# Kernel tuning notes

Hardware: AMD Instinct MI355X
Metric: run time of the kernel (lower is better)

The kernel has to match this reference:

```python
import jax, jax.numpy as jnp
import numpy as np
import math

HIDDEN = 2048
N_HEADS = 16
N_KV = 8
HEAD_DIM = 128
EPS = 1e-6
THETA = 1000000.0
B, S = 1, 2048


def rotate_half(x):
    x1, x2 = jnp.split(x, 2, axis=-1)
    return jnp.concatenate((-x2, x1), axis=-1)


def rms_norm(x, w, eps=EPS):
    xf = x.astype(jnp.float32)
    var = jnp.mean(xf * xf, axis=-1, keepdims=True)
    return (w * (xf * jax.lax.rsqrt(var + eps)).astype(x.dtype))


def setup_inputs() -> dict:
    key = jax.random.key(0)
    ks = jax.random.split(key, 8)
    hidden_states = jax.random.normal(ks[0], (B, S, HIDDEN), dtype=jnp.float32)
    # additive causal mask: 0 on/below diagonal, -1e9 above
    causal = jnp.triu(jnp.full((S, S), -1e9, dtype=jnp.float32), k=1)
    attention_mask = causal[None, None, :, :]
    position_ids = jnp.arange(S, dtype=jnp.int64 if jax.config.jax_enable_x64 else jnp.int32)[None, :]
    sc = 0.02
    wq = jax.random.normal(ks[1], (N_HEADS * HEAD_DIM, HIDDEN), dtype=jnp.float32) * sc
    wk = jax.random.normal(ks[2], (N_KV * HEAD_DIM, HIDDEN), dtype=jnp.float32) * sc
    wv = jax.random.normal(ks[3], (N_KV * HEAD_DIM, HIDDEN), dtype=jnp.float32) * sc
    wo = jax.random.normal(ks[4], (HIDDEN, N_HEADS * HEAD_DIM), dtype=jnp.float32) * sc
    q_norm_w = jnp.ones((HEAD_DIM,), dtype=jnp.float32)
    k_norm_w = jnp.ones((HEAD_DIM,), dtype=jnp.float32)
    return {"hidden_states": hidden_states, "attention_mask": attention_mask,
            "position_ids": position_ids, "wq": wq, "wk": wk, "wv": wv,
            "wo": wo, "q_norm_w": q_norm_w, "k_norm_w": k_norm_w}


def reference(hidden_states, attention_mask, position_ids, wq, wk, wv, wo, q_norm_w, k_norm_w):
    b, s, _ = hidden_states.shape
    # projections (nn.Linear: x @ W^T)
    q = (hidden_states @ wq.T).reshape(b, s, N_HEADS, HEAD_DIM).transpose(0, 2, 1, 3)   # [b,h,s,d]
    k = (hidden_states @ wk.T).reshape(b, s, N_KV, HEAD_DIM).transpose(0, 2, 1, 3)      # [b,kv,s,d]
    v = (hidden_states @ wv.T).reshape(b, s, N_KV, HEAD_DIM).transpose(0, 2, 1, 3)
    # rotary embedding
    inv_freq = 1.0 / (THETA ** (jnp.arange(0, HEAD_DIM, 2, dtype=jnp.float32) / HEAD_DIM))  # [d/2]
    freqs = position_ids.astype(jnp.float32)[:, :, None] * inv_freq[None, None, :]          # [b,s,d/2]
    emb = jnp.concatenate((freqs, freqs), axis=-1)                                          # [b,s,d]
    cos = jnp.cos(emb)[:, None, :, :].astype(hidden_states.dtype)                           # [b,1,s,d]
    sin = jnp.sin(emb)[:, None, :, :].astype(hidden_states.dtype)
    q = q * cos + rotate_half(q) * sin
    k = k * cos + rotate_half(k) * sin
    # per-head QK RMSNorm (applied AFTER RoPE, matching source)
    q = rms_norm(q, q_norm_w)
    k = rms_norm(k, k_norm_w)
    # GQA repeat kv heads
    n_rep = N_HEADS // N_KV
    k = jnp.repeat(k, n_rep, axis=1)  # [b,h,s,d]
    v = jnp.repeat(v, n_rep, axis=1)
    # attention
    scores = jnp.einsum('bhqd,bhkd->bhqk', q, k) / math.sqrt(HEAD_DIM)
    scores = scores + attention_mask
    probs = jax.nn.softmax(scores.astype(jnp.float32), axis=-1).astype(q.dtype)
    ctx = jnp.einsum('bhqk,bhkd->bhqd', probs, v)
    ctx = ctx.transpose(0, 2, 1, 3).reshape(b, s, N_HEADS * HEAD_DIM)
    return ctx @ wo.T
```

## Files before the change

kernel.cpp:

```cpp
#include <hip/hip_runtime.h>
#include <hip/hip_bf16.h>

#define HIDDEN   2048
#define N_HEADS  16
#define N_KV     8
#define HEAD_DIM 128
#define SEQ      2048
#define EPS      1e-6f

#define BM 128
#define BN 128
#define BK 32

#define ATQ 64
#define ATK 64
#define QKS 136
#define VTS 72

typedef __hip_bfloat16 bf16;
typedef __bf16  bf16x8 __attribute__((ext_vector_type(8)));
typedef short   short8 __attribute__((ext_vector_type(8)));
typedef short   short4v __attribute__((ext_vector_type(4)));
typedef float   f32x4  __attribute__((ext_vector_type(4)));

typedef __attribute__((address_space(1))) void gvoid;
typedef __attribute__((address_space(3))) void lvoid;

#define ASYNC16(g, l) \
    __builtin_amdgcn_global_load_lds((gvoid*)(g), (lvoid*)(l), 16, 0, 0)

__device__ __forceinline__ short f2bfbits(float x) {
    union { bf16 h; short s; } u;
    u.h = __float2bfloat16(x);
    return u.s;
}

__global__ __launch_bounds__(256) void cvt_bf16(const float4* __restrict__ src,
                                                short4v* __restrict__ dst, int n4) {
    const int i = blockIdx.x * 256 + threadIdx.x;
    if (i >= n4) return;
    const float4 v = src[i];
    short4v p;
    p[0] = f2bfbits(v.x); p[1] = f2bfbits(v.y);
    p[2] = f2bfbits(v.z); p[3] = f2bfbits(v.w);
    dst[i] = p;
}

template <int MODE>
__device__ __forceinline__ void gemm_bf(const bf16* __restrict__ A,
                                        const bf16* __restrict__ B,
                                        float* __restrict__ C,
                                        bf16* __restrict__ Ct,
                                        int K, int ldc, int bm, int bn) {
    __shared__ __align__(16) short As[BM * BK];
    __shared__ __align__(16) short Bs[BN * BK];
    const int tid  = threadIdx.x;
    const int lane = tid & 63;
    const int wave = tid >> 6;
    const int wy   = wave & 1;
    const int wx   = wave >> 1;
    const int lrow = lane & 15;
    const int lk   = lane >> 4;
    const int srow = tid >> 2;
    const int scol = (tid & 3) * 8;

    f32x4 acc[4][4] = {};

    for (int k0 = 0; k0 < K; k0 += BK) {
        #pragma unroll
        for (int r = 0; r < 2; r++) {
            const int row = r * 64 + srow;
            ASYNC16(&A[(size_t)(bm + row) * K + k0 + scol],
                    &As[(r * 64 + wave * 16) * BK]);
            ASYNC16(&B[(size_t)(bn + row) * K + k0 + scol],
                    &Bs[(r * 64 + wave * 16) * BK]);
        }
        __syncthreads();

        short8 af[4], bfr[4];
        #pragma unroll
        for (int i = 0; i < 4; i++) {
            af[i]  = *(const short8*)&As[(wy * 64 + i * 16 + lrow) * BK + lk * 8];
            bfr[i] = *(const short8*)&Bs[(wx * 64 + i * 16 + lrow) * BK + lk * 8];
        }
        #pragma unroll
        for (int i = 0; i < 4; i++)
            #pragma unroll
            for (int j = 0; j < 4; j++)
                acc[i][j] = __builtin_amdgcn_mfma_f32_16x16x32_bf16(
                    __builtin_bit_cast(bf16x8, af[i]),
                    __builtin_bit_cast(bf16x8, bfr[j]), acc[i][j], 0, 0, 0);
        __syncthreads();
    }

    #pragma unroll
    for (int i = 0; i < 4; i++)
        #pragma unroll
        for (int j = 0; j < 4; j++) {
            if (MODE == 0) {
                #pragma unroll
                for (int v = 0; v < 4; v++)
                    C[(size_t)(bm + wy * 64 + i * 16 + lk * 4 + v) * ldc
                      + bn + wx * 64 + j * 16 + lrow] = acc[i][j][v];
            } else {
                short4v pk;
                #pragma unroll
                for (int v = 0; v < 4; v++) pk[v] = f2bfbits(acc[i][j][v]);
                *(short4v*)&Ct[(size_t)(bn + wx * 64 + j * 16 + lrow) * ldc
                               + bm + wy * 64 + i * 16 + lk * 4] = pk;
            }
        }
}

__global__ __launch_bounds__(256) void qkv_mfma(const bf16* __restrict__ x,
                                                const bf16* __restrict__ wq,
                                                const bf16* __restrict__ wk,
                                                const bf16* __restrict__ wv,
                                                float* __restrict__ Q,
                                                float* __restrict__ Kc,
                                                bf16* __restrict__ Vt) {
    const int by = blockIdx.y;
    const int bm = blockIdx.x * 128;
    if (by < 16)
        gemm_bf<0>(x, wq, Q, nullptr, HIDDEN, 2048, bm, by * 128);
    else if (by < 24)
        gemm_bf<0>(x, wk, Kc, nullptr, HIDDEN, 1024, bm, (by - 16) * 128);
    else
        gemm_bf<1>(x, wv, nullptr, Vt, HIDDEN, SEQ, bm, (by - 24) * 128);
}

__global__ __launch_bounds__(256) void oproj_mfma(const bf16* __restrict__ ctx,
                                                  const bf16* __restrict__ wo,
                                                  float* __restrict__ out) {
    gemm_bf<0>(ctx, wo, out, nullptr, N_HEADS * HEAD_DIM, HIDDEN,
               blockIdx.x * 128, blockIdx.y * 128);
}

__global__ __launch_bounds__(256) void rope_norm_kernel(
        const float* __restrict__ Q, const float* __restrict__ K,
        bf16* __restrict__ Qbf, bf16* __restrict__ Kbf,
        const float* __restrict__ qw, const float* __restrict__ kw) {
    const int s = blockIdx.x;
    const int h = blockIdx.y * 4 + (threadIdx.x >> 6);
    const int l = threadIdx.x & 63;

    const float* src;
    const float* w;
    if (h < N_HEADS) { src = Q + (size_t)s * (N_HEADS * HEAD_DIM) + h * HEAD_DIM; w = qw; }
    else             { src = K + (size_t)s * (N_KV * HEAD_DIM) + (h - N_HEADS) * HEAD_DIM; w = kw; }

    const float x1 = src[l];
    const float x2 = src[l + 64];
    const float inv_freq = exp2f((float)l * (-19.931568569324174f / 64.0f));
    const float ang = (float)s * inv_freq;
    float sn, cs;
    __sincosf(ang, &sn, &cs);
    float r1 = x1 * cs - x2 * sn;
    float r2 = x2 * cs + x1 * sn;

    float ss = r1 * r1 + r2 * r2;
    #pragma unroll
    for (int off = 1; off < 64; off <<= 1)
        ss += __shfl_xor(ss, off, 64);
    const float rs = rsqrtf(ss / 128.0f + EPS);

    if (h < N_HEADS) {
        bf16* dst = Qbf + ((size_t)s * N_HEADS + h) * HEAD_DIM;
        dst[l]      = __float2bfloat16(w[l] * r1 * rs);
        dst[l + 64] = __float2bfloat16(w[l + 64] * r2 * rs);
    } else {
        bf16* dst = Kbf + ((size_t)s * N_KV + (h - N_HEADS)) * HEAD_DIM;
        dst[l]      = __float2bfloat16(w[l] * r1 * rs);
        dst[l + 64] = __float2bfloat16(w[l + 64] * r2 * rs);
    }
}

__global__ __launch_bounds__(256) void attn_mfma(bf16* __restrict__ QC,
                                                 const bf16* __restrict__ KbfG,
                                                 const bf16* __restrict__ VtG) {
    const int h     = blockIdx.y;
    const int px    = (int)((blockIdx.x * 13u) & 31u);
    const int qtile = (h < 8) ? px : 31 - px;
    const int q0    = qtile * ATQ;
    const int kvh   = h >> 1;
    const int tid   = threadIdx.x;
    const int lane  = tid & 63;
    const int w     = tid >> 6;
    const int lrow  = lane & 15;
    const int lk    = lane >> 4;
    const float scale = 0.08838834764831845f;

    __shared__ short Ks[ATK * QKS];
    __shared__ short Vt[HEAD_DIM * VTS];
    __shared__ short Ps[ATQ * VTS];

    f32x4 O[8] = {};
    float m_run[4] = {-1e30f, -1e30f, -1e30f, -1e30f};
    float l_run[4] = {};

    short8 aq[4];
    {
        const bf16* qrow =
            &QC[(size_t)(q0 + w * 16 + lrow) * (N_HEADS * HEAD_DIM) + h * HEAD_DIM];
        #pragma unroll
        for (int kc = 0; kc < 4; kc++)
            aq[kc] = *(const short8*)&qrow[kc * 32 + lk * 8];
    }

    for (int t = 0; t <= qtile; t++) {
        const int k0 = t * ATK;
        for (int idx = tid; idx < ATK * 16; idx += 256) {
            const int r = idx >> 4, c8 = idx & 15;
            *(short8*)&Ks[r * QKS + c8 * 8] = *(const short8*)
                &KbfG[((size_t)(k0 + r) * N_KV + kvh) * HEAD_DIM + c8 * 8];
        }
        for (int idx = tid; idx < HEAD_DIM * 8; idx += 256) {
            const int d = idx >> 3, ck = idx & 7;
            *(short8*)&Vt[d * VTS + ck * 8] =
                *(const short8*)&VtG[((size_t)kvh * HEAD_DIM + d) * SEQ + k0 + ck * 8];
        }
        __syncthreads();

        f32x4 s[4] = {};
        #pragma unroll
        for (int nt = 0; nt < 4; nt++)
            #pragma unroll
            for (int kc = 0; kc < 4; kc++) {
                const short8 bk = *(const short8*)
                    &Ks[(nt * 16 + lrow) * QKS + kc * 32 + lk * 8];
                s[nt] = __builtin_amdgcn_mfma_f32_16x16x32_bf16(
                    __builtin_bit_cast(bf16x8, aq[kc]),
                    __builtin_bit_cast(bf16x8, bk), s[nt], 0, 0, 0);
            }

        float p[4][4];
        float mloc[4] = {-1e30f, -1e30f, -1e30f, -1e30f};
        #pragma unroll
        for (int nt = 0; nt < 4; nt++) {
            const int kglob = k0 + nt * 16 + lrow;
            #pragma unroll
            for (int r = 0; r < 4; r++) {
                float v = s[nt][r] * scale;
                v = (kglob <= q0 + w * 16 + lk * 4 + r) ? v : -1e30f;
                p[nt][r] = v;
                mloc[r] = fmaxf(mloc[r], v);
            }
        }
        #pragma unroll
        for (int off = 1; off < 16; off <<= 1)
            #pragma unroll
            for (int r = 0; r < 4; r++)
                mloc[r] = fmaxf(mloc[r], __shfl_xor(mloc[r], off, 64));

        float alpha[4], ls[4];
        #pragma unroll
        for (int r = 0; r < 4; r++) {
            const float mnew = fmaxf(m_run[r], mloc[r]);
            alpha[r] = __expf(m_run[r] - mnew);
            m_run[r] = mnew;
            ls[r] = 0.f;
        }
        #pragma unroll
        for (int nt = 0; nt < 4; nt++)
            #pragma unroll
            for (int r = 0; r < 4; r++) {
                const float e = __expf(p[nt][r] - m_run[r]);
                Ps[(w * 16 + lk * 4 + r) * VTS + nt * 16 + lrow] = f2bfbits(e);
                ls[r] += e;
            }
        #pragma unroll
        for (int off = 1; off < 16; off <<= 1)
            #pragma unroll
            for (int r = 0; r < 4; r++)
                ls[r] += __shfl_xor(ls[r], off, 64);
        #pragma unroll
        for (int r = 0; r < 4; r++)
            l_run[r] = l_run[r] * alpha[r] + ls[r];
        #pragma unroll
        for (int dnt = 0; dnt < 8; dnt++)
            #pragma unroll
            for (int r = 0; r < 4; r++)
                O[dnt][r] *= alpha[r];

        __syncthreads();

        short8 pa[2];
        #pragma unroll
        for (int ks = 0; ks < 2; ks++)
            pa[ks] = *(const short8*)&Ps[(w * 16 + lrow) * VTS + ks * 32 + lk * 8];
        #pragma unroll
        for (int dnt = 0; dnt < 8; dnt++)
            #pragma unroll
            for (int ks = 0; ks < 2; ks++) {
                const short8 vb = *(const short8*)
                    &Vt[(dnt * 16 + lrow) * VTS + ks * 32 + lk * 8];
                O[dnt] = __builtin_amdgcn_mfma_f32_16x16x32_bf16(
                    __builtin_bit_cast(bf16x8, pa[ks]),
                    __builtin_bit_cast(bf16x8, vb), O[dnt], 0, 0, 0);
            }
        __syncthreads();
    }

    #pragma unroll
    for (int r = 0; r < 4; r++) {
        const float invl = 1.0f / l_run[r];
        bf16* orow = &QC[(size_t)(q0 + w * 16 + lk * 4 + r) * (N_HEADS * HEAD_DIM)
                         + h * HEAD_DIM];
        #pragma unroll
        for (int dnt = 0; dnt < 8; dnt++)
            orow[dnt * 16 + lrow] = __float2bfloat16(O[dnt][r] * invl);
    }
}

extern "C" void kernel_launch(void* const* d_in, const int* in_sizes, int n_in,
                              void* d_out, int out_size, void* d_ws, size_t ws_size,
                              hipStream_t stream) {
    const float* x   = (const float*)d_in[0];
    const float* wq  = (const float*)d_in[3];
    const float* wk  = (const float*)d_in[4];
    const float* wv  = (const float*)d_in[5];
    const float* wo  = (const float*)d_in[6];
    const float* qnw = (const float*)d_in[7];
    const float* knw = (const float*)d_in[8];

    char*  ws   = (char*)d_ws;
    float* Qw   = (float*)ws;
    bf16*  xbf  = (bf16*)(ws + (16u << 20));
    bf16*  wqbf = (bf16*)(ws + (24u << 20));
    bf16*  wobf = wqbf;
    bf16*  wkbf = (bf16*)(ws + (32u << 20));
    bf16*  wvbf = (bf16*)(ws + (36u << 20));
    bf16*  Qbf  = (bf16*)(ws + (40u << 20));
    float* Kb   = (float*)d_out;
    bf16*  VtG  = (bf16*)((char*)d_out + (8u << 20));
    bf16*  KbfG = (bf16*)((char*)d_out + (12u << 20));

    cvt_bf16<<<4096, 256, 0, stream>>>((const float4*)x,  (short4v*)xbf,  1048576);
    cvt_bf16<<<4096, 256, 0, stream>>>((const float4*)wq, (short4v*)wqbf, 1048576);
    cvt_bf16<<<2048, 256, 0, stream>>>((const float4*)wk, (short4v*)wkbf, 524288);
    cvt_bf16<<<2048, 256, 0, stream>>>((const float4*)wv, (short4v*)wvbf, 524288);

    qkv_mfma<<<dim3(SEQ / 128, 32), 256, 0, stream>>>(xbf, wqbf, wkbf, wvbf,
                                                      Qw, Kb, VtG);

    cvt_bf16<<<4096, 256, 0, stream>>>((const float4*)wo, (short4v*)wobf, 1048576);

    rope_norm_kernel<<<dim3(SEQ, 6), 256, 0, stream>>>(Qw, Kb, Qbf, KbfG, qnw, knw);

    attn_mfma<<<dim3(SEQ / ATQ, N_HEADS), 256, 0, stream>>>(Qbf, KbfG, VtG);

    oproj_mfma<<<dim3(SEQ / 128, HIDDEN / 128), 256, 0, stream>>>(Qbf, wobf,
                                                                  (float*)d_out);
}
```

Baseline: 375.4 us.

## Split causal attention over KV range for long query tiles and combine partials

Query tiles in the second half of the sequence now have their KV loop split into two chunks handled by separate blocks, giving 48 blocks per head instead of 32 with a max of 16 KV tiles each. Each block writes unnormalized fp32 partial outputs plus running max and sum, and a new combine kernel merges them with log-sum-exp rescaling and writes bf16 context. This targets the load imbalance and tail of the causal attention grid, at the cost of an extra launch and fp32 partial-output traffic through the workspace.

```diff
diff --git a/kernel.cpp b/kernel.cpp
--- a/kernel.cpp
+++ b/kernel.cpp
@@ -16,6 +16,7 @@
 #define ATK 64
 #define QKS 136
 #define VTS 72
+#define CHUNK 16
 
 typedef __hip_bfloat16 bf16;
 typedef __bf16  bf16x8 __attribute__((ext_vector_type(8)));
@@ -175,12 +176,17 @@
     }
 }
 
-__global__ __launch_bounds__(256) void attn_mfma(bf16* __restrict__ QC,
-                                                 const bf16* __restrict__ KbfG,
-                                                 const bf16* __restrict__ VtG) {
-    const int h     = blockIdx.y;
-    const int px    = (int)((blockIdx.x * 13u) & 31u);
-    const int qtile = (h < 8) ? px : 31 - px;
+__global__ __launch_bounds__(256) void attn_split(const bf16* __restrict__ QC,
+                                                  const bf16* __restrict__ KbfG,
+                                                  const bf16* __restrict__ VtG,
+                                                  float* __restrict__ Opart,
+                                                  float* __restrict__ Ml) {
+    const int h  = blockIdx.y;
+    const int bx = blockIdx.x;
+    int qtile, t0, t1;
+    if (bx < 16)      { qtile = bx;                 t0 = 0;  t1 = qtile; }
+    else { const int idx = bx - 16; qtile = 16 + (idx >> 1);
+           if (idx & 1) { t0 = 16; t1 = qtile; } else { t0 = 0; t1 = 15; } }
     const int q0    = qtile * ATQ;
     const int kvh   = h >> 1;
     const int tid   = threadIdx.x;
@@ -207,7 +213,7 @@
             aq[kc] = *(const short8*)&qrow[kc * 32 + lk * 8];
     }
 
-    for (int t = 0; t <= qtile; t++) {
+    for (int t = t0; t <= t1; t++) {
         const int k0 = t * ATK;
         for (int idx = tid; idx < ATK * 16; idx += 256) {
             const int r = idx >> 4, c8 = idx & 15;
@@ -301,15 +307,60 @@
         __syncthreads();
     }
 
+    const int slot = h * 48 + bx;
     #pragma unroll
     for (int r = 0; r < 4; r++) {
-        const float invl = 1.0f / l_run[r];
-        bf16* orow = &QC[(size_t)(q0 + w * 16 + lk * 4 + r) * (N_HEADS * HEAD_DIM)
-                         + h * HEAD_DIM];
+        const int row = w * 16 + lk * 4 + r;
+        float* orow = &Opart[(size_t)slot * (ATQ * HEAD_DIM) + row * HEAD_DIM];
         #pragma unroll
         for (int dnt = 0; dnt < 8; dnt++)
-            orow[dnt * 16 + lrow] = __float2bfloat16(O[dnt][r] * invl);
-    }
+            orow[dnt * 16 + lrow] = O[dnt][r];
+        if (lrow == 0) {
+            Ml[slot * (ATQ * 2) + row * 2]     = m_run[r];
+            Ml[slot * (ATQ * 2) + row * 2 + 1] = l_run[r];
+        }
+    }
+}
+
+__global__ __launch_bounds__(256) void attn_combine(const float* __restrict__ Opart,
+                                                    const float* __restrict__ Ml,
+                                                    bf16* __restrict__ Qbf) {
+    const int h   = blockIdx.y;
+    const int s   = blockIdx.x * 8 + (threadIdx.x >> 5);
+    const int d   = (threadIdx.x & 31) * 4;
+    const int qt  = s >> 6;
+    const int row = s & 63;
+
+    int slot0, nch;
+    if (qt < 16) { slot0 = h * 48 + qt;                 nch = 1; }
+    else         { slot0 = h * 48 + 16 + 2 * (qt - 16); nch = 2; }
+
+    const float m0 = Ml[slot0 * (ATQ * 2) + row * 2];
+    const float l0 = Ml[slot0 * (ATQ * 2) + row * 2 + 1];
+    float4 o = *(const float4*)&Opart[(size_t)slot0 * (ATQ * HEAD_DIM)
+                                      + row * HEAD_DIM + d];
+    float L;
+    if (nch == 2) {
+        const float m1 = Ml[(slot0 + 1) * (ATQ * 2) + row * 2];
+        const float l1 = Ml[(slot0 + 1) * (ATQ * 2) + row * 2 + 1];
+        const float4 o1 = *(const float4*)&Opart[(size_t)(slot0 + 1) * (ATQ * HEAD_DIM)
+                                                 + row * HEAD_DIM + d];
+        const float M  = fmaxf(m0, m1);
+        const float e0 = __expf(m0 - M);
+        const float e1 = __expf(m1 - M);
+        L = l0 * e0 + l1 * e1;
+        o.x = o.x * e0 + o1.x * e1;
+        o.y = o.y * e0 + o1.y * e1;
+        o.z = o.z * e0 + o1.z * e1;
+        o.w = o.w * e0 + o1.w * e1;
+    } else {
+        L = l0;
+    }
+    const float inv = 1.0f / L;
+    short4v pk;
+    pk[0] = f2bfbits(o.x * inv); pk[1] = f2bfbits(o.y * inv);
+    pk[2] = f2bfbits(o.z * inv); pk[3] = f2bfbits(o.w * inv);
+    *(short4v*)&Qbf[((size_t)s * N_HEADS + h) * HEAD_DIM + d] = pk;
 }
 
 extern "C" void kernel_launch(void* const* d_in, const int* in_sizes, int n_in,
@@ -323,17 +374,19 @@
     const float* qnw = (const float*)d_in[7];
     const float* knw = (const float*)d_in[8];
 
-    char*  ws   = (char*)d_ws;
-    float* Qw   = (float*)ws;
-    bf16*  xbf  = (bf16*)(ws + (16u << 20));
-    bf16*  wqbf = (bf16*)(ws + (24u << 20));
-    bf16*  wobf = wqbf;
-    bf16*  wkbf = (bf16*)(ws + (32u << 20));
-    bf16*  wvbf = (bf16*)(ws + (36u << 20));
-    bf16*  Qbf  = (bf16*)(ws + (40u << 20));
-    float* Kb   = (float*)d_out;
-    bf16*  VtG  = (bf16*)((char*)d_out + (8u << 20));
-    bf16*  KbfG = (bf16*)((char*)d_out + (12u << 20));
+    char*  ws    = (char*)d_ws;
+    float* Qw    = (float*)ws;
+    bf16*  xbf   = (bf16*)(ws + (16u << 20));
+    bf16*  wqbf  = (bf16*)(ws + (24u << 20));
+    bf16*  wobf  = wqbf;
+    bf16*  wkbf  = (bf16*)(ws + (32u << 20));
+    bf16*  wvbf  = (bf16*)(ws + (36u << 20));
+    bf16*  Qbf   = (bf16*)(ws + (40u << 20));
+    float* Opart = (float*)ws;
+    float* Ml    = (float*)(ws + (32u << 20));
+    float* Kb    = (float*)d_out;
+    bf16*  VtG   = (bf16*)((char*)d_out + (8u << 20));
+    bf16*  KbfG  = (bf16*)((char*)d_out + (12u << 20));
 
     cvt_bf16<<<4096, 256, 0, stream>>>((const float4*)x,  (short4v*)xbf,  1048576);
     cvt_bf16<<<4096, 256, 0, stream>>>((const float4*)wq, (short4v*)wqbf, 1048576);
@@ -347,7 +400,9 @@
 
     rope_norm_kernel<<<dim3(SEQ, 6), 256, 0, stream>>>(Qw, Kb, Qbf, KbfG, qnw, knw);
 
-    attn_mfma<<<dim3(SEQ / ATQ, N_HEADS), 256, 0, stream>>>(Qbf, KbfG, VtG);
+    attn_split<<<dim3(48, N_HEADS), 256, 0, stream>>>(Qbf, KbfG, VtG, Opart, Ml);
+
+    attn_combine<<<dim3(SEQ / 8, N_HEADS), 256, 0, stream>>>(Opart, Ml, Qbf);
 
     oproj_mfma<<<dim3(SEQ / 128, HIDDEN / 128), 256, 0, stream>>>(Qbf, wobf,
                                                                   (float*)d_out);
```

Result: faster. 322.8 us (-14.0%).
